# Kernel tuning notes

Measured on AMD Instinct MI355X. Metric: run time of the kernel, lower is better.

The kernel has to match this reference:

```python
import jax, jax.numpy as jnp
import numpy as np

NUM_HEADS = 16

def setup_inputs() -> dict:
    key = jax.random.key(0)
    k1, k2, k3 = jax.random.split(key, 3)
    D = 1024
    return {
        "hidden_states": jax.random.normal(k1, (2, 2048, D), dtype=jnp.float32),
        "c_attn_w": jax.random.normal(k2, (D, 3 * D), dtype=jnp.float32) * 0.02,
        "c_attn_b": jnp.zeros((3 * D,), dtype=jnp.float32),
        "c_proj_w": jax.random.normal(k3, (D, D), dtype=jnp.float32) * 0.02,
        "c_proj_b": jnp.zeros((D,), dtype=jnp.float32),
    }

def reference(hidden_states, c_attn_w, c_attn_b, c_proj_w, c_proj_b):
    B, S, D = hidden_states.shape
    H = NUM_HEADS
    hd = D // H
    # Conv1D: x @ W + b, then split into q, k, v
    qkv = hidden_states @ c_attn_w + c_attn_b  # [B, S, 3D]
    q, k, v = jnp.split(qkv, 3, axis=-1)
    q = q.reshape(B, S, H, hd).transpose(0, 2, 1, 3)  # [B, H, S, hd]
    k = k.reshape(B, S, H, hd).transpose(0, 2, 1, 3)
    v = v.reshape(B, S, H, hd).transpose(0, 2, 1, 3)
    # scaled QK^T
    scores = jnp.einsum("bhqd,bhkd->bhqk", q, k) / jnp.asarray(hd ** 0.5, q.dtype)
    # causal mask (tril), masked positions set to dtype min per original code
    causal = jnp.tril(jnp.ones((S, S), dtype=bool))
    mask_value = jnp.finfo(scores.dtype).min
    scores = jnp.where(causal[None, None], scores, mask_value)
    attn = jax.nn.softmax(scores, axis=-1)
    out = jnp.einsum("bhqk,bhkd->bhqd", attn, v)  # [B, H, S, hd]
    out = out.transpose(0, 2, 1, 3).reshape(B, S, D)
    out = out @ c_proj_w + c_proj_b
    return out
```

## Files before the change

kernel.cpp:

```cpp
#include <hip/hip_runtime.h>
#include <math.h>

#define B_ 2
#define S_ 2048
#define D_ 1024
#define H_ 16
#define HD 64
#define M_ (B_ * S_)
#define N_QKV (3 * D_)

typedef short short8 __attribute__((ext_vector_type(8)));
typedef float floatx4 __attribute__((ext_vector_type(4)));

static __device__ __forceinline__ unsigned short f2bf_rne(float x) {
    union { float f; unsigned u; } v; v.f = x;
    unsigned r = v.u + 0x7FFFu + ((v.u >> 16) & 1u);
    return (unsigned short)(r >> 16);
}
static __device__ __forceinline__ float bf2f(unsigned short b) {
    union { unsigned u; float f; } v; v.u = ((unsigned)b) << 16;
    return v.f;
}
static __device__ __forceinline__ void split2(float x, unsigned short& h, unsigned short& l) {
    h = f2bf_rne(x);
    l = f2bf_rne(x - bf2f(h));
}

static __device__ __forceinline__ void dma16(const void* g, void* l) {
    __builtin_amdgcn_global_load_lds(
        (const __attribute__((address_space(1))) unsigned int*)g,
        (__attribute__((address_space(3))) unsigned int*)l,
        16, 0, 0);
}

__global__ __launch_bounds__(256) void prep_wT(
    const float* __restrict__ W, int N,
    unsigned short* __restrict__ Thi, unsigned short* __restrict__ Tlo)
{
    __shared__ float Ws[64][68];
    const int t  = threadIdx.x;
    const int n0 = blockIdx.x * 64, k0 = blockIdx.y * 64;
    {
        const int kl = t >> 4, nl = (t & 15) * 4;
        const float* src = W + (size_t)(k0 + kl) * N + n0 + nl;
#pragma unroll
        for (int g = 0; g < 4; g++)
            *(float4*)&Ws[kl + g * 16][nl] = *(const float4*)(src + (size_t)g * 16 * N);
    }
    __syncthreads();
    {
        const int nl = t >> 2, ks = (t & 3) * 16;
        short8 h0, h1, l0, l1;
#pragma unroll
        for (int j = 0; j < 8; j++) {
            unsigned short hh, ll;
            split2(Ws[ks + j][nl], hh, ll);
            h0[j] = (short)hh; l0[j] = (short)ll;
        }
#pragma unroll
        for (int j = 0; j < 8; j++) {
            unsigned short hh, ll;
            split2(Ws[ks + 8 + j][nl], hh, ll);
            h1[j] = (short)hh; l1[j] = (short)ll;
        }
        unsigned short* dh = Thi + (size_t)(n0 + nl) * D_ + k0 + ks;
        unsigned short* dl = Tlo + (size_t)(n0 + nl) * D_ + k0 + ks;
        *(short8*)dh = h0; *(short8*)(dh + 8) = h1;
        *(short8*)dl = l0; *(short8*)(dl + 8) = l1;
    }
}

__global__ __launch_bounds__(256) void gemm_qkv(
    const float* __restrict__ A,
    const unsigned short* __restrict__ BThi, const unsigned short* __restrict__ BTlo,
    const float* __restrict__ bias,
    unsigned short* __restrict__ Qhi, unsigned short* __restrict__ Qlo,
    unsigned short* __restrict__ Khi, unsigned short* __restrict__ Klo,
    unsigned short* __restrict__ vThi, unsigned short* __restrict__ vTlo)
{
    __shared__ unsigned short sAh[128 * 32], sAl[128 * 32];
    __shared__ unsigned short sBh[128 * 32], sBl[128 * 32];

    const int t    = threadIdx.x;
    const int m0   = blockIdx.y * 128, n0 = blockIdx.x * 128;
    const int lane = t & 63, wave = t >> 6;
    const int lm   = lane & 15, quad = lane >> 4;
    const int wm   = (wave >> 1) * 64, wn = (wave & 1) * 64;

    const int srow = t >> 1, sseg = (t & 1) * 16;
    const float* Ap = A + (size_t)(m0 + srow) * D_ + sseg;

    const int lrow = lane >> 2, lcol = (lane & 3) * 8;
    const unsigned short* gBh0 = BThi + (size_t)(n0 + wave * 32 + lrow) * D_ + lcol;
    const unsigned short* gBl0 = BTlo + (size_t)(n0 + wave * 32 + lrow) * D_ + lcol;
    unsigned short* lBh0 = sBh + wave * 1024 + lane * 8;
    unsigned short* lBl0 = sBl + wave * 1024 + lane * 8;

    floatx4 acc[4][4];
#pragma unroll
    for (int i = 0; i < 4; i++)
#pragma unroll
        for (int j = 0; j < 4; j++)
#pragma unroll
            for (int r = 0; r < 4; r++) acc[i][j][r] = 0.f;

    float4 af[4];
    af[0] = *(const float4*)(Ap);     af[1] = *(const float4*)(Ap + 4);
    af[2] = *(const float4*)(Ap + 8); af[3] = *(const float4*)(Ap + 12);

    for (int k0 = 0; k0 < D_; k0 += 32) {
        short8 ah0, ah1, al0, al1;
#pragma unroll
        for (int g = 0; g < 4; g++) {
            float xs[4] = {af[g].x, af[g].y, af[g].z, af[g].w};
#pragma unroll
            for (int e = 0; e < 4; e++) {
                unsigned short hh, ll;
                split2(xs[e], hh, ll);
                if (g < 2) { ah0[g * 4 + e] = (short)hh; al0[g * 4 + e] = (short)ll; }
                else       { ah1[(g - 2) * 4 + e] = (short)hh; al1[(g - 2) * 4 + e] = (short)ll; }
            }
        }
        __syncthreads();
        {
            unsigned short* a = &sAh[srow * 32 + sseg];
            unsigned short* b = &sAl[srow * 32 + sseg];
            *(short8*)a = ah0; *(short8*)(a + 8) = ah1;
            *(short8*)b = al0; *(short8*)(b + 8) = al1;
        }
        dma16(gBh0 + k0, lBh0);
        dma16(gBh0 + (size_t)16 * D_ + k0, lBh0 + 512);
        dma16(gBl0 + k0, lBl0);
        dma16(gBl0 + (size_t)16 * D_ + k0, lBl0 + 512);
        __syncthreads();

        if (k0 + 32 < D_) {
            const float* an = Ap + k0 + 32;
            af[0] = *(const float4*)(an);     af[1] = *(const float4*)(an + 4);
            af[2] = *(const float4*)(an + 8); af[3] = *(const float4*)(an + 12);
        }

        short8 bhf[4], blf[4];
#pragma unroll
        for (int nb = 0; nb < 4; nb++) {
            const int r = wn + nb * 16 + lm;
            bhf[nb] = *(const short8*)&sBh[r * 32 + quad * 8];
            blf[nb] = *(const short8*)&sBl[r * 32 + quad * 8];
        }
#pragma unroll
        for (int mb = 0; mb < 4; mb++) {
            const int r = wm + mb * 16 + lm;
            short8 ah = *(const short8*)&sAh[r * 32 + quad * 8];
            short8 al = *(const short8*)&sAl[r * 32 + quad * 8];
#pragma unroll
            for (int nb = 0; nb < 4; nb++) {
                acc[mb][nb] = __builtin_amdgcn_mfma_f32_16x16x32_bf16(ah, bhf[nb], acc[mb][nb], 0, 0, 0);
                acc[mb][nb] = __builtin_amdgcn_mfma_f32_16x16x32_bf16(al, bhf[nb], acc[mb][nb], 0, 0, 0);
                acc[mb][nb] = __builtin_amdgcn_mfma_f32_16x16x32_bf16(ah, blf[nb], acc[mb][nb], 0, 0, 0);
            }
        }
    }

    const int nmode = n0 >> 10;
    if (nmode == 0) {
#pragma unroll
        for (int nb = 0; nb < 4; nb++) {
            const int c = n0 + wn + nb * 16 + lm;
            const float bv = bias[c];
#pragma unroll
            for (int mb = 0; mb < 4; mb++) {
                const int rowb = m0 + wm + mb * 16 + quad * 4;
#pragma unroll
                for (int r = 0; r < 4; r++) {
                    unsigned short hh, ll;
                    split2((acc[mb][nb][r] + bv) * 0.125f, hh, ll);
                    Qhi[(size_t)(rowb + r) * D_ + c] = hh;
                    Qlo[(size_t)(rowb + r) * D_ + c] = ll;
                }
            }
        }
    } else if (nmode == 1) {
#pragma unroll
        for (int nb = 0; nb < 4; nb++) {
            const int c = n0 + wn + nb * 16 + lm;
            const float bv = bias[c];
            const int cq = c - 1024;
#pragma unroll
            for (int mb = 0; mb < 4; mb++) {
                const int rowb = m0 + wm + mb * 16 + quad * 4;
#pragma unroll
                for (int r = 0; r < 4; r++) {
                    unsigned short hh, ll;
                    split2(acc[mb][nb][r] + bv, hh, ll);
                    Khi[(size_t)(rowb + r) * D_ + cq] = hh;
                    Klo[(size_t)(rowb + r) * D_ + cq] = ll;
                }
            }
        }
    } else {
#pragma unroll
        for (int nb = 0; nb < 4; nb++) {
            const int c = n0 + wn + nb * 16 + lm;
            const float bv = bias[c];
            const int cq = c - 2048;
            const int hh_ = cq >> 6, dd = cq & 63;
#pragma unroll
            for (int mb = 0; mb < 4; mb++) {
                const int rowb = m0 + wm + mb * 16 + quad * 4;
                const int bb = rowb >> 11, ss = rowb & 2047;
                unsigned short hv[4], lv[4];
#pragma unroll
                for (int r = 0; r < 4; r++)
                    split2(acc[mb][nb][r] + bv, hv[r], lv[r]);
                const size_t idx = ((size_t)((bb * 16 + hh_) * 64 + dd)) * S_ + ss;
                *(uint2*)&vThi[idx] = make_uint2((unsigned)hv[0] | ((unsigned)hv[1] << 16),
                                                 (unsigned)hv[2] | ((unsigned)hv[3] << 16));
                *(uint2*)&vTlo[idx] = make_uint2((unsigned)lv[0] | ((unsigned)lv[1] << 16),
                                                 (unsigned)lv[2] | ((unsigned)lv[3] << 16));
            }
        }
    }
}

__global__ __launch_bounds__(256) void gemm_out(
    const unsigned short* __restrict__ Ahi, const unsigned short* __restrict__ Alo,
    const unsigned short* __restrict__ BThi, const unsigned short* __restrict__ BTlo,
    const float* __restrict__ bias, float* __restrict__ C)
{
    __shared__ unsigned short sAh[64 * 32], sAl[64 * 32];
    __shared__ unsigned short sBh[64 * 32], sBl[64 * 32];

    const int t    = threadIdx.x;
    const int m0   = blockIdx.y * 64, n0 = blockIdx.x * 64;
    const int lane = t & 63, wave = t >> 6;
    const int lm   = lane & 15, quad = lane >> 4;

    const int lrow = lane >> 2, lcol = (lane & 3) * 8;
    const unsigned short* gAh = Ahi + (size_t)(m0 + wave * 16 + lrow) * D_ + lcol;
    const unsigned short* gAl = Alo + (size_t)(m0 + wave * 16 + lrow) * D_ + lcol;
    const unsigned short* gBh = BThi + (size_t)(n0 + wave * 16 + lrow) * D_ + lcol;
    const unsigned short* gBl = BTlo + (size_t)(n0 + wave * 16 + lrow) * D_ + lcol;
    unsigned short* lAh = sAh + wave * 512 + lane * 8;
    unsigned short* lAl = sAl + wave * 512 + lane * 8;
    unsigned short* lBh = sBh + wave * 512 + lane * 8;
    unsigned short* lBl = sBl + wave * 512 + lane * 8;

    floatx4 acc[4];
#pragma unroll
    for (int j = 0; j < 4; j++)
#pragma unroll
        for (int r = 0; r < 4; r++) acc[j][r] = 0.f;

    for (int k0 = 0; k0 < D_; k0 += 32) {
        __syncthreads();
        dma16(gAh + k0, lAh);
        dma16(gAl + k0, lAl);
        dma16(gBh + k0, lBh);
        dma16(gBl + k0, lBl);
        __syncthreads();

        short8 ah = *(const short8*)&sAh[(wave * 16 + lm) * 32 + quad * 8];
        short8 al = *(const short8*)&sAl[(wave * 16 + lm) * 32 + quad * 8];
#pragma unroll
        for (int nb = 0; nb < 4; nb++) {
            short8 bh = *(const short8*)&sBh[(nb * 16 + lm) * 32 + quad * 8];
            short8 bl = *(const short8*)&sBl[(nb * 16 + lm) * 32 + quad * 8];
            acc[nb] = __builtin_amdgcn_mfma_f32_16x16x32_bf16(ah, bh, acc[nb], 0, 0, 0);
            acc[nb] = __builtin_amdgcn_mfma_f32_16x16x32_bf16(al, bh, acc[nb], 0, 0, 0);
            acc[nb] = __builtin_amdgcn_mfma_f32_16x16x32_bf16(ah, bl, acc[nb], 0, 0, 0);
        }
    }

#pragma unroll
    for (int nb = 0; nb < 4; nb++) {
        const int col = n0 + nb * 16 + lm;
        const float bv = bias[col];
#pragma unroll
        for (int r = 0; r < 4; r++) {
            const int row = m0 + wave * 16 + quad * 4 + r;
            C[(size_t)row * D_ + col] = acc[nb][r] + bv;
        }
    }
}

#define PST 72

__global__ __launch_bounds__(512, 4) void flash_attn_mfma(
    unsigned short* QAhi, unsigned short* QAlo,
    const unsigned short* __restrict__ Khi, const unsigned short* __restrict__ Klo,
    const unsigned short* __restrict__ vThi, const unsigned short* __restrict__ vTlo)
{
    __shared__ unsigned short KhiS[64 * PST];
    __shared__ unsigned short KloS[64 * PST];
    __shared__ unsigned short VhiS[64 * PST];
    __shared__ unsigned short VloS[64 * PST];
    __shared__ unsigned short PhS[128 * PST];
    __shared__ unsigned short PlS[128 * PST];

    const int t    = threadIdx.x;
    const int pj   = blockIdx.x;
    const int bh   = blockIdx.y;
    const int b    = bh >> 4, h = bh & 15;
    const int lane = t & 63, w = t >> 6;
    const int lm   = lane & 15, quad = lane >> 4;

    const int srow = t >> 3;
    const int sseg = (t & 7) * 8;

    const unsigned short* Kh_b = Khi + (size_t)(b * S_) * D_ + h * HD + sseg;
    const unsigned short* Kl_b = Klo + (size_t)(b * S_) * D_ + h * HD + sseg;
    const unsigned short* Vh_b = vThi + ((size_t)((b * 16 + h) * 64 + srow)) * S_ + sseg;
    const unsigned short* Vl_b = vTlo + ((size_t)((b * 16 + h) * 64 + srow)) * S_ + sseg;

    for (int phse = 0; phse < 2; phse++) {
        const int qt = phse ? (15 - pj) : pj;
        const int q0 = qt * 128;
        const int ntiles = 2 * qt + 2;
        const int wdiag = (q0 >> 6) + (w >> 2);

        short8 qh[2], ql[2];
        {
            const size_t qoff = (size_t)(b * S_ + q0 + 16 * w + lm) * D_ + h * HD + quad * 8;
            qh[0] = *(const short8*)&QAhi[qoff];
            qh[1] = *(const short8*)&QAhi[qoff + 32];
            ql[0] = *(const short8*)&QAlo[qoff];
            ql[1] = *(const short8*)&QAlo[qoff + 32];
        }

        float lsum[4] = {0.f, 0.f, 0.f, 0.f};
        floatx4 o[4];
#pragma unroll
        for (int nb = 0; nb < 4; nb++)
#pragma unroll
            for (int r = 0; r < 4; r++) o[nb][r] = 0.f;

        uint4 pkh, pkl, pvh, pvl;
        pkh = *(const uint4*)(Kh_b + (size_t)srow * D_);
        pkl = *(const uint4*)(Kl_b + (size_t)srow * D_);
        pvh = *(const uint4*)(Vh_b);
        pvl = *(const uint4*)(Vl_b);

        for (int kt = 0; kt < ntiles; kt++) {
            __syncthreads();
            *(uint4*)&KhiS[srow * PST + sseg] = pkh;
            *(uint4*)&KloS[srow * PST + sseg] = pkl;
            *(uint4*)&VhiS[srow * PST + sseg] = pvh;
            *(uint4*)&VloS[srow * PST + sseg] = pvl;
            __syncthreads();

            if (kt + 1 < ntiles) {
                const int k1 = (kt + 1) * 64;
                pkh = *(const uint4*)(Kh_b + (size_t)(k1 + srow) * D_);
                pkl = *(const uint4*)(Kl_b + (size_t)(k1 + srow) * D_);
                pvh = *(const uint4*)(Vh_b + k1);
                pvl = *(const uint4*)(Vl_b + k1);
            }

            if (kt <= wdiag) {
                floatx4 sa[4];
#pragma unroll
                for (int nb = 0; nb < 4; nb++)
#pragma unroll
                    for (int r = 0; r < 4; r++) sa[nb][r] = 0.f;
#pragma unroll
                for (int s = 0; s < 2; s++) {
#pragma unroll
                    for (int nb = 0; nb < 4; nb++) {
                        short8 kh = *(const short8*)&KhiS[(nb * 16 + lm) * PST + s * 32 + quad * 8];
                        short8 kl = *(const short8*)&KloS[(nb * 16 + lm) * PST + s * 32 + quad * 8];
                        sa[nb] = __builtin_amdgcn_mfma_f32_16x16x32_bf16(qh[s], kh, sa[nb], 0, 0, 0);
                        sa[nb] = __builtin_amdgcn_mfma_f32_16x16x32_bf16(ql[s], kh, sa[nb], 0, 0, 0);
                        sa[nb] = __builtin_amdgcn_mfma_f32_16x16x32_bf16(qh[s], kl, sa[nb], 0, 0, 0);
                    }
                }

                const bool diag = (kt == wdiag);
                const int kbase = kt * 64;
#pragma unroll
                for (int r = 0; r < 4; r++) {
                    const int qabs = q0 + 16 * w + 4 * quad + r;
                    const int rloc = 16 * w + 4 * quad + r;
#pragma unroll
                    for (int nb = 0; nb < 4; nb++) {
                        float p = __expf(sa[nb][r]);
                        if (diag && (kbase + 16 * nb + lm > qabs)) p = 0.f;
                        lsum[r] += p;
                        unsigned short hh, ll;
                        split2(p, hh, ll);
                        PhS[rloc * PST + 16 * nb + lm] = hh;
                        PlS[rloc * PST + 16 * nb + lm] = ll;
                    }
                }

#pragma unroll
                for (int ks = 0; ks < 2; ks++) {
                    short8 pf = *(const short8*)&PhS[(16 * w + lm) * PST + ks * 32 + quad * 8];
                    short8 pg = *(const short8*)&PlS[(16 * w + lm) * PST + ks * 32 + quad * 8];
#pragma unroll
                    for (int nb = 0; nb < 4; nb++) {
                        short8 vhf = *(const short8*)&VhiS[(16 * nb + lm) * PST + ks * 32 + quad * 8];
                        short8 vlf = *(const short8*)&VloS[(16 * nb + lm) * PST + ks * 32 + quad * 8];
                        o[nb] = __builtin_amdgcn_mfma_f32_16x16x32_bf16(pf, vhf, o[nb], 0, 0, 0);
                        o[nb] = __builtin_amdgcn_mfma_f32_16x16x32_bf16(pg, vhf, o[nb], 0, 0, 0);
                        o[nb] = __builtin_amdgcn_mfma_f32_16x16x32_bf16(pf, vlf, o[nb], 0, 0, 0);
                    }
                }
            }
        }

#pragma unroll
        for (int r = 0; r < 4; r++) {
            float l = lsum[r];
            l += __shfl_xor(l, 1);
            l += __shfl_xor(l, 2);
            l += __shfl_xor(l, 4);
            l += __shfl_xor(l, 8);
            const float inv = 1.f / l;
            const size_t rowoff =
                (size_t)(b * S_ + q0 + 16 * w + 4 * quad + r) * D_ + h * HD + lm;
#pragma unroll
            for (int nb = 0; nb < 4; nb++) {
                unsigned short hh, ll;
                split2(o[nb][r] * inv, hh, ll);
                QAhi[rowoff + 16 * nb] = hh;
                QAlo[rowoff + 16 * nb] = ll;
            }
        }
    }
}

extern "C" void kernel_launch(void* const* d_in, const int* in_sizes, int n_in,
                              void* d_out, int out_size, void* d_ws, size_t ws_size,
                              hipStream_t stream)
{
    const float* hs     = (const float*)d_in[0];
    const float* attn_w = (const float*)d_in[1];
    const float* attn_b = (const float*)d_in[2];
    const float* proj_w = (const float*)d_in[3];
    const float* proj_b = (const float*)d_in[4];
    float* outp = (float*)d_out;

    const size_t QE = (size_t)M_ * D_;
    const size_t WQ = (size_t)D_ * N_QKV;
    unsigned short* Qhi   = (unsigned short*)d_ws;
    unsigned short* Qlo   = Qhi + QE;
    unsigned short* Khi   = Qlo + QE;
    unsigned short* Klo   = Khi + QE;
    unsigned short* vThi  = Klo + QE;
    unsigned short* vTlo  = vThi + QE;
    unsigned short* WqThi = vTlo + QE;
    unsigned short* WqTlo = WqThi + WQ;
    unsigned short* WpThi = WqTlo + WQ;
    unsigned short* WpTlo = WpThi + (size_t)D_ * D_;

    dim3 blk(256);
    prep_wT<<<dim3(N_QKV / 64, D_ / 64), blk, 0, stream>>>(attn_w, N_QKV, WqThi, WqTlo);
    prep_wT<<<dim3(D_ / 64, D_ / 64), blk, 0, stream>>>(proj_w, D_, WpThi, WpTlo);
    gemm_qkv<<<dim3(N_QKV / 128, M_ / 128), blk, 0, stream>>>(
        hs, WqThi, WqTlo, attn_b, Qhi, Qlo, Khi, Klo, vThi, vTlo);
    flash_attn_mfma<<<dim3(8, B_ * H_), dim3(512), 0, stream>>>(
        Qhi, Qlo, Khi, Klo, vThi, vTlo);
    gemm_out<<<dim3(D_ / 64, M_ / 64), blk, 0, stream>>>(
        Qhi, Qlo, WpThi, WpTlo, proj_b, outp);
}
```

Before: 315.9 us.

## Pre-split activations, retile flash attention to 64-row tiles, swizzle output GEMM blocks

Several changes at once. A new prep_A kernel splits the fp32 hidden states into bf16 hi/lo arrays once, so gemm_qkv loads A by direct global-to-LDS DMA instead of converting in its main loop. Flash attention drops from 128-query tiles with 512 threads to 64-query tiles with 256 threads, doubles the grid, removes the per-wave diagonal skip, and raises wave priority around the MFMA sections. gemm_out uses a 1D grid with a block-index swizzle for cache locality, and bf16 conversion now uses the library intrinsic. The cost is an extra kernel launch plus a written and re-read activation buffer in workspace.

```diff
diff --git a/kernel.cpp b/kernel.cpp
--- a/kernel.cpp
+++ b/kernel.cpp
@@ -1,4 +1,5 @@
 #include <hip/hip_runtime.h>
+#include <hip/hip_bf16.h>
 #include <math.h>
 
 #define B_ 2
@@ -12,18 +13,19 @@
 typedef short short8 __attribute__((ext_vector_type(8)));
 typedef float floatx4 __attribute__((ext_vector_type(4)));
 
-static __device__ __forceinline__ unsigned short f2bf_rne(float x) {
-    union { float f; unsigned u; } v; v.f = x;
-    unsigned r = v.u + 0x7FFFu + ((v.u >> 16) & 1u);
-    return (unsigned short)(r >> 16);
+static __device__ __forceinline__ unsigned short f2bf(float x) {
+    __hip_bfloat16 h = __float2bfloat16(x);
+    unsigned short u;
+    __builtin_memcpy(&u, &h, sizeof(u));
+    return u;
 }
 static __device__ __forceinline__ float bf2f(unsigned short b) {
     union { unsigned u; float f; } v; v.u = ((unsigned)b) << 16;
     return v.f;
 }
 static __device__ __forceinline__ void split2(float x, unsigned short& h, unsigned short& l) {
-    h = f2bf_rne(x);
-    l = f2bf_rne(x - bf2f(h));
+    h = f2bf(x);
+    l = f2bf(x - bf2f(h));
 }
 
 static __device__ __forceinline__ void dma16(const void* g, void* l) {
@@ -31,6 +33,25 @@
         (const __attribute__((address_space(1))) unsigned int*)g,
         (__attribute__((address_space(3))) unsigned int*)l,
         16, 0, 0);
+}
+
+__global__ __launch_bounds__(256) void prep_A(
+    const float* __restrict__ X,
+    unsigned short* __restrict__ Ahi, unsigned short* __restrict__ Alo)
+{
+    const size_t i = ((size_t)blockIdx.x * 256 + threadIdx.x) * 8;
+    float4 a = *(const float4*)(X + i);
+    float4 b = *(const float4*)(X + i + 4);
+    float xs[8] = {a.x, a.y, a.z, a.w, b.x, b.y, b.z, b.w};
+    short8 h, l;
+#pragma unroll
+    for (int e = 0; e < 8; e++) {
+        unsigned short hh, ll;
+        split2(xs[e], hh, ll);
+        h[e] = (short)hh; l[e] = (short)ll;
+    }
+    *(short8*)&Ahi[i] = h;
+    *(short8*)&Alo[i] = l;
 }
 
 __global__ __launch_bounds__(256) void prep_wT(
@@ -71,7 +92,7 @@
 }
 
 __global__ __launch_bounds__(256) void gemm_qkv(
-    const float* __restrict__ A,
+    const unsigned short* __restrict__ Ahi, const unsigned short* __restrict__ Alo,
     const unsigned short* __restrict__ BThi, const unsigned short* __restrict__ BTlo,
     const float* __restrict__ bias,
     unsigned short* __restrict__ Qhi, unsigned short* __restrict__ Qlo,
@@ -87,14 +108,12 @@
     const int lm   = lane & 15, quad = lane >> 4;
     const int wm   = (wave >> 1) * 64, wn = (wave & 1) * 64;
 
-    const int srow = t >> 1, sseg = (t & 1) * 16;
-    const float* Ap = A + (size_t)(m0 + srow) * D_ + sseg;
-
     const int lrow = lane >> 2, lcol = (lane & 3) * 8;
-    const unsigned short* gBh0 = BThi + (size_t)(n0 + wave * 32 + lrow) * D_ + lcol;
-    const unsigned short* gBl0 = BTlo + (size_t)(n0 + wave * 32 + lrow) * D_ + lcol;
-    unsigned short* lBh0 = sBh + wave * 1024 + lane * 8;
-    unsigned short* lBl0 = sBl + wave * 1024 + lane * 8;
+    const unsigned short* gAh = Ahi + (size_t)(m0 + wave * 32 + lrow) * D_ + lcol;
+    const unsigned short* gAl = Alo + (size_t)(m0 + wave * 32 + lrow) * D_ + lcol;
+    const unsigned short* gBh = BThi + (size_t)(n0 + wave * 32 + lrow) * D_ + lcol;
+    const unsigned short* gBl = BTlo + (size_t)(n0 + wave * 32 + lrow) * D_ + lcol;
+    const int ldst = wave * 1024 + lane * 8;
 
     floatx4 acc[4][4];
 #pragma unroll
@@ -104,41 +123,17 @@
 #pragma unroll
             for (int r = 0; r < 4; r++) acc[i][j][r] = 0.f;
 
-    float4 af[4];
-    af[0] = *(const float4*)(Ap);     af[1] = *(const float4*)(Ap + 4);
-    af[2] = *(const float4*)(Ap + 8); af[3] = *(const float4*)(Ap + 12);
-
     for (int k0 = 0; k0 < D_; k0 += 32) {
-        short8 ah0, ah1, al0, al1;
-#pragma unroll
-        for (int g = 0; g < 4; g++) {
-            float xs[4] = {af[g].x, af[g].y, af[g].z, af[g].w};
-#pragma unroll
-            for (int e = 0; e < 4; e++) {
-                unsigned short hh, ll;
-                split2(xs[e], hh, ll);
-                if (g < 2) { ah0[g * 4 + e] = (short)hh; al0[g * 4 + e] = (short)ll; }
-                else       { ah1[(g - 2) * 4 + e] = (short)hh; al1[(g - 2) * 4 + e] = (short)ll; }
-            }
-        }
         __syncthreads();
-        {
-            unsigned short* a = &sAh[srow * 32 + sseg];
-            unsigned short* b = &sAl[srow * 32 + sseg];
-            *(short8*)a = ah0; *(short8*)(a + 8) = ah1;
-            *(short8*)b = al0; *(short8*)(b + 8) = al1;
-        }
-        dma16(gBh0 + k0, lBh0);
-        dma16(gBh0 + (size_t)16 * D_ + k0, lBh0 + 512);
-        dma16(gBl0 + k0, lBl0);
-        dma16(gBl0 + (size_t)16 * D_ + k0, lBl0 + 512);
+        dma16(gAh + k0, &sAh[ldst]);
+        dma16(gAh + (size_t)16 * D_ + k0, &sAh[ldst + 512]);
+        dma16(gAl + k0, &sAl[ldst]);
+        dma16(gAl + (size_t)16 * D_ + k0, &sAl[ldst + 512]);
+        dma16(gBh + k0, &sBh[ldst]);
+        dma16(gBh + (size_t)16 * D_ + k0, &sBh[ldst + 512]);
+        dma16(gBl + k0, &sBl[ldst]);
+        dma16(gBl + (size_t)16 * D_ + k0, &sBl[ldst + 512]);
         __syncthreads();
-
-        if (k0 + 32 < D_) {
-            const float* an = Ap + k0 + 32;
-            af[0] = *(const float4*)(an);     af[1] = *(const float4*)(an + 4);
-            af[2] = *(const float4*)(an + 8); af[3] = *(const float4*)(an + 12);
-        }
 
         short8 bhf[4], blf[4];
 #pragma unroll
@@ -230,8 +225,11 @@
     __shared__ unsigned short sAh[64 * 32], sAl[64 * 32];
     __shared__ unsigned short sBh[64 * 32], sBl[64 * 32];
 
-    const int t    = threadIdx.x;
-    const int m0   = blockIdx.y * 64, n0 = blockIdx.x * 64;
+    const int t   = threadIdx.x;
+    const int lid = blockIdx.x;
+    const int swz = (lid & 7) * 128 + (lid >> 3);
+    const int bx  = swz & 15, by = swz >> 4;
+    const int m0  = by * 64, n0 = bx * 64;
     const int lane = t & 63, wave = t >> 6;
     const int lm   = lane & 15, quad = lane >> 4;
 
@@ -285,17 +283,14 @@
 
 #define PST 72
 
-__global__ __launch_bounds__(512, 4) void flash_attn_mfma(
+__global__ __launch_bounds__(256, 2) void flash_attn_mfma(
     unsigned short* QAhi, unsigned short* QAlo,
     const unsigned short* __restrict__ Khi, const unsigned short* __restrict__ Klo,
     const unsigned short* __restrict__ vThi, const unsigned short* __restrict__ vTlo)
 {
-    __shared__ unsigned short KhiS[64 * PST];
-    __shared__ unsigned short KloS[64 * PST];
-    __shared__ unsigned short VhiS[64 * PST];
-    __shared__ unsigned short VloS[64 * PST];
-    __shared__ unsigned short PhS[128 * PST];
-    __shared__ unsigned short PlS[128 * PST];
+    __shared__ unsigned short KhS[64 * PST], KlS[64 * PST];
+    __shared__ unsigned short VhS[64 * PST], VlS[64 * PST];
+    __shared__ unsigned short PhS[64 * PST], PlS[64 * PST];
 
     const int t    = threadIdx.x;
     const int pj   = blockIdx.x;
@@ -304,19 +299,20 @@
     const int lane = t & 63, w = t >> 6;
     const int lm   = lane & 15, quad = lane >> 4;
 
-    const int srow = t >> 3;
-    const int sseg = (t & 7) * 8;
+    const int srow = t >> 2;
+    const int sseg = (t & 3) * 16;
 
     const unsigned short* Kh_b = Khi + (size_t)(b * S_) * D_ + h * HD + sseg;
     const unsigned short* Kl_b = Klo + (size_t)(b * S_) * D_ + h * HD + sseg;
     const unsigned short* Vh_b = vThi + ((size_t)((b * 16 + h) * 64 + srow)) * S_ + sseg;
     const unsigned short* Vl_b = vTlo + ((size_t)((b * 16 + h) * 64 + srow)) * S_ + sseg;
 
+    const int sdst = srow * PST + sseg;
+
     for (int phse = 0; phse < 2; phse++) {
-        const int qt = phse ? (15 - pj) : pj;
-        const int q0 = qt * 128;
-        const int ntiles = 2 * qt + 2;
-        const int wdiag = (q0 >> 6) + (w >> 2);
+        const int qt = phse ? (31 - pj) : pj;
+        const int q0 = qt * 64;
+        const int ntiles = qt + 1;
 
         short8 qh[2], ql[2];
         {
@@ -334,78 +330,88 @@
 #pragma unroll
             for (int r = 0; r < 4; r++) o[nb][r] = 0.f;
 
-        uint4 pkh, pkl, pvh, pvl;
-        pkh = *(const uint4*)(Kh_b + (size_t)srow * D_);
-        pkl = *(const uint4*)(Kl_b + (size_t)srow * D_);
-        pvh = *(const uint4*)(Vh_b);
-        pvl = *(const uint4*)(Vl_b);
+        uint4 pkh0, pkh1, pkl0, pkl1, pvh0, pvh1, pvl0, pvl1;
+        pkh0 = *(const uint4*)(Kh_b + (size_t)srow * D_);
+        pkh1 = *(const uint4*)(Kh_b + (size_t)srow * D_ + 8);
+        pkl0 = *(const uint4*)(Kl_b + (size_t)srow * D_);
+        pkl1 = *(const uint4*)(Kl_b + (size_t)srow * D_ + 8);
+        pvh0 = *(const uint4*)(Vh_b);
+        pvh1 = *(const uint4*)(Vh_b + 8);
+        pvl0 = *(const uint4*)(Vl_b);
+        pvl1 = *(const uint4*)(Vl_b + 8);
 
         for (int kt = 0; kt < ntiles; kt++) {
             __syncthreads();
-            *(uint4*)&KhiS[srow * PST + sseg] = pkh;
-            *(uint4*)&KloS[srow * PST + sseg] = pkl;
-            *(uint4*)&VhiS[srow * PST + sseg] = pvh;
-            *(uint4*)&VloS[srow * PST + sseg] = pvl;
+            *(uint4*)&KhS[sdst] = pkh0; *(uint4*)&KhS[sdst + 8] = pkh1;
+            *(uint4*)&KlS[sdst] = pkl0; *(uint4*)&KlS[sdst + 8] = pkl1;
+            *(uint4*)&VhS[sdst] = pvh0; *(uint4*)&VhS[sdst + 8] = pvh1;
+            *(uint4*)&VlS[sdst] = pvl0; *(uint4*)&VlS[sdst + 8] = pvl1;
             __syncthreads();
 
             if (kt + 1 < ntiles) {
                 const int k1 = (kt + 1) * 64;
-                pkh = *(const uint4*)(Kh_b + (size_t)(k1 + srow) * D_);
-                pkl = *(const uint4*)(Kl_b + (size_t)(k1 + srow) * D_);
-                pvh = *(const uint4*)(Vh_b + k1);
-                pvl = *(const uint4*)(Vl_b + k1);
-            }
-
-            if (kt <= wdiag) {
-                floatx4 sa[4];
-#pragma unroll
-                for (int nb = 0; nb < 4; nb++)
-#pragma unroll
-                    for (int r = 0; r < 4; r++) sa[nb][r] = 0.f;
-#pragma unroll
-                for (int s = 0; s < 2; s++) {
-#pragma unroll
-                    for (int nb = 0; nb < 4; nb++) {
-                        short8 kh = *(const short8*)&KhiS[(nb * 16 + lm) * PST + s * 32 + quad * 8];
-                        short8 kl = *(const short8*)&KloS[(nb * 16 + lm) * PST + s * 32 + quad * 8];
-                        sa[nb] = __builtin_amdgcn_mfma_f32_16x16x32_bf16(qh[s], kh, sa[nb], 0, 0, 0);
-                        sa[nb] = __builtin_amdgcn_mfma_f32_16x16x32_bf16(ql[s], kh, sa[nb], 0, 0, 0);
-                        sa[nb] = __builtin_amdgcn_mfma_f32_16x16x32_bf16(qh[s], kl, sa[nb], 0, 0, 0);
-                    }
+                pkh0 = *(const uint4*)(Kh_b + (size_t)(k1 + srow) * D_);
+                pkh1 = *(const uint4*)(Kh_b + (size_t)(k1 + srow) * D_ + 8);
+                pkl0 = *(const uint4*)(Kl_b + (size_t)(k1 + srow) * D_);
+                pkl1 = *(const uint4*)(Kl_b + (size_t)(k1 + srow) * D_ + 8);
+                pvh0 = *(const uint4*)(Vh_b + k1);
+                pvh1 = *(const uint4*)(Vh_b + k1 + 8);
+                pvl0 = *(const uint4*)(Vl_b + k1);
+                pvl1 = *(const uint4*)(Vl_b + k1 + 8);
+            }
+
+            floatx4 sa[4];
+#pragma unroll
+            for (int nb = 0; nb < 4; nb++)
+#pragma unroll
+                for (int r = 0; r < 4; r++) sa[nb][r] = 0.f;
+            __builtin_amdgcn_s_setprio(1);
+#pragma unroll
+            for (int s = 0; s < 2; s++) {
+#pragma unroll
+                for (int nb = 0; nb < 4; nb++) {
+                    short8 kh = *(const short8*)&KhS[(nb * 16 + lm) * PST + s * 32 + quad * 8];
+                    short8 kl = *(const short8*)&KlS[(nb * 16 + lm) * PST + s * 32 + quad * 8];
+                    sa[nb] = __builtin_amdgcn_mfma_f32_16x16x32_bf16(qh[s], kh, sa[nb], 0, 0, 0);
+                    sa[nb] = __builtin_amdgcn_mfma_f32_16x16x32_bf16(ql[s], kh, sa[nb], 0, 0, 0);
+                    sa[nb] = __builtin_amdgcn_mfma_f32_16x16x32_bf16(qh[s], kl, sa[nb], 0, 0, 0);
                 }
-
-                const bool diag = (kt == wdiag);
-                const int kbase = kt * 64;
-#pragma unroll
-                for (int r = 0; r < 4; r++) {
-                    const int qabs = q0 + 16 * w + 4 * quad + r;
-                    const int rloc = 16 * w + 4 * quad + r;
-#pragma unroll
-                    for (int nb = 0; nb < 4; nb++) {
-                        float p = __expf(sa[nb][r]);
-                        if (diag && (kbase + 16 * nb + lm > qabs)) p = 0.f;
-                        lsum[r] += p;
-                        unsigned short hh, ll;
-                        split2(p, hh, ll);
-                        PhS[rloc * PST + 16 * nb + lm] = hh;
-                        PlS[rloc * PST + 16 * nb + lm] = ll;
-                    }
+            }
+            __builtin_amdgcn_s_setprio(0);
+
+            const bool diag = (kt == qt);
+            const int kbase = kt * 64;
+#pragma unroll
+            for (int r = 0; r < 4; r++) {
+                const int qabs = q0 + 16 * w + 4 * quad + r;
+                const int rloc = 16 * w + 4 * quad + r;
+#pragma unroll
+                for (int nb = 0; nb < 4; nb++) {
+                    float p = __expf(sa[nb][r]);
+                    if (diag && (kbase + 16 * nb + lm > qabs)) p = 0.f;
+                    lsum[r] += p;
+                    unsigned short hh, ll;
+                    split2(p, hh, ll);
+                    PhS[rloc * PST + 16 * nb + lm] = hh;
+                    PlS[rloc * PST + 16 * nb + lm] = ll;
                 }
-
-#pragma unroll
-                for (int ks = 0; ks < 2; ks++) {
-                    short8 pf = *(const short8*)&PhS[(16 * w + lm) * PST + ks * 32 + quad * 8];
-                    short8 pg = *(const short8*)&PlS[(16 * w + lm) * PST + ks * 32 + quad * 8];
-#pragma unroll
-                    for (int nb = 0; nb < 4; nb++) {
-                        short8 vhf = *(const short8*)&VhiS[(16 * nb + lm) * PST + ks * 32 + quad * 8];
-                        short8 vlf = *(const short8*)&VloS[(16 * nb + lm) * PST + ks * 32 + quad * 8];
-                        o[nb] = __builtin_amdgcn_mfma_f32_16x16x32_bf16(pf, vhf, o[nb], 0, 0, 0);
-                        o[nb] = __builtin_amdgcn_mfma_f32_16x16x32_bf16(pg, vhf, o[nb], 0, 0, 0);
-                        o[nb] = __builtin_amdgcn_mfma_f32_16x16x32_bf16(pf, vlf, o[nb], 0, 0, 0);
-                    }
+            }
+
+            __builtin_amdgcn_s_setprio(1);
+#pragma unroll
+            for (int ks = 0; ks < 2; ks++) {
+                short8 pf = *(const short8*)&PhS[(16 * w + lm) * PST + ks * 32 + quad * 8];
+                short8 pg = *(const short8*)&PlS[(16 * w + lm) * PST + ks * 32 + quad * 8];
+#pragma unroll
+                for (int nb = 0; nb < 4; nb++) {
+                    short8 vhf = *(const short8*)&VhS[(16 * nb + lm) * PST + ks * 32 + quad * 8];
+                    short8 vlf = *(const short8*)&VlS[(16 * nb + lm) * PST + ks * 32 + quad * 8];
+                    o[nb] = __builtin_amdgcn_mfma_f32_16x16x32_bf16(pf, vhf, o[nb], 0, 0, 0);
+                    o[nb] = __builtin_amdgcn_mfma_f32_16x16x32_bf16(pg, vhf, o[nb], 0, 0, 0);
+                    o[nb] = __builtin_amdgcn_mfma_f32_16x16x32_bf16(pf, vlf, o[nb], 0, 0, 0);
                 }
             }
+            __builtin_amdgcn_s_setprio(0);
         }
 
 #pragma unroll
@@ -452,14 +458,17 @@
     unsigned short* WqTlo = WqThi + WQ;
     unsigned short* WpThi = WqTlo + WQ;
     unsigned short* WpTlo = WpThi + (size_t)D_ * D_;
+    unsigned short* Ahi   = WpTlo + (size_t)D_ * D_;
+    unsigned short* Alo   = Ahi + QE;
 
     dim3 blk(256);
+    prep_A<<<dim3(M_ * D_ / 2048), blk, 0, stream>>>(hs, Ahi, Alo);
     prep_wT<<<dim3(N_QKV / 64, D_ / 64), blk, 0, stream>>>(attn_w, N_QKV, WqThi, WqTlo);
     prep_wT<<<dim3(D_ / 64, D_ / 64), blk, 0, stream>>>(proj_w, D_, WpThi, WpTlo);
     gemm_qkv<<<dim3(N_QKV / 128, M_ / 128), blk, 0, stream>>>(
-        hs, WqThi, WqTlo, attn_b, Qhi, Qlo, Khi, Klo, vThi, vTlo);
-    flash_attn_mfma<<<dim3(8, B_ * H_), dim3(512), 0, stream>>>(
+        Ahi, Alo, WqThi, WqTlo, attn_b, Qhi, Qlo, Khi, Klo, vThi, vTlo);
+    flash_attn_mfma<<<dim3(16, B_ * H_), dim3(256), 0, stream>>>(
         Qhi, Qlo, Khi, Klo, vThi, vTlo);
-    gemm_out<<<dim3(D_ / 64, M_ / 64), blk, 0, stream>>>(
+    gemm_out<<<dim3(1024), blk, 0, stream>>>(
         Qhi, Qlo, WpThi, WpTlo, proj_b, outp);
 }
```

Result: no change. 316.3 us (+0.1%).
